# Performance work log

Hardware: AMD Instinct MI355X
Metric: run time of the kernel (lower is better)

The kernel has to match this reference:

```python
import jax, jax.numpy as jnp
import numpy as np

INPUT_DIM = 128
HIDDEN_DIM = 256
TOP_K = 512
M = 8192
N = 8192


def setup_inputs() -> dict:
    key = jax.random.key(0)
    ks = jax.random.split(key, 10)
    s_in = 1.0 / np.sqrt(INPUT_DIM)
    s_h = 1.0 / np.sqrt(HIDDEN_DIM)
    return {
        "desc0": jax.random.normal(ks[0], (1, M, INPUT_DIM), jnp.float32),
        "desc1": jax.random.normal(ks[1], (1, N, INPUT_DIM), jnp.float32),
        # mlpc0: Linear(in,h) -> ReLU -> Linear(h,h); weights stored [in,out]
        "W0a": jax.random.uniform(ks[2], (INPUT_DIM, HIDDEN_DIM), jnp.float32, -s_in, s_in),
        "b0a": jax.random.uniform(ks[3], (HIDDEN_DIM,), jnp.float32, -s_in, s_in),
        "W0b": jax.random.uniform(ks[4], (HIDDEN_DIM, HIDDEN_DIM), jnp.float32, -s_h, s_h),
        "b0b": jax.random.uniform(ks[5], (HIDDEN_DIM,), jnp.float32, -s_h, s_h),
        "W1a": jax.random.uniform(ks[6], (INPUT_DIM, HIDDEN_DIM), jnp.float32, -s_in, s_in),
        "b1a": jax.random.uniform(ks[7], (HIDDEN_DIM,), jnp.float32, -s_in, s_in),
        "W1b": jax.random.uniform(ks[8], (HIDDEN_DIM, HIDDEN_DIM), jnp.float32, -s_h, s_h),
        "b1b": jax.random.uniform(ks[9], (HIDDEN_DIM,), jnp.float32, -s_h, s_h),
    }


def _mlp(x, Wa, ba, Wb, bb):
    h = jax.nn.relu(x @ Wa + ba)
    return h @ Wb + bb


def reference(desc0, desc1, W0a, b0a, W0b, b0b, W1a, b1a, W1b, b1b):
    mdesc0 = _mlp(desc0, W0a, b0a, W0b, b0b)  # [1, M, H]
    mdesc1 = _mlp(desc1, W1a, b1a, W1b, b1b)  # [1, N, H]
    sim = jnp.einsum("bmd,bnd->bmn", mdesc0, mdesc1)  # [1, M, N]
    flat = sim[0].reshape(-1)
    _, top_idx = jax.lax.top_k(flat, TOP_K)
    n = sim.shape[2]
    rows = top_idx // n
    cols = top_idx % n
    top_k_indices_2d = jnp.stack([rows, cols], axis=1)  # [TOP_K, 2]
    return top_k_indices_2d, sim
```

## Files before the change

### kernel.cpp

```cpp
#include <hip/hip_runtime.h>
#include <stdint.h>

#define H_DIM 256
#define NCOL 8192
#define TOPK 512
#define CAND_CAP 8192

typedef unsigned short u16;
typedef __attribute__((ext_vector_type(8))) __bf16 bf16x8;
typedef __attribute__((ext_vector_type(4))) float f32x4;
typedef unsigned __attribute__((address_space(3))) lds_u32;
typedef const unsigned __attribute__((address_space(1))) glb_u32;

__device__ __forceinline__ unsigned fkey(float f) {
  unsigned u = __float_as_uint(f);
  unsigned m = (unsigned)((int)u >> 31) | 0x80000000u;
  return u ^ m;
}

__device__ __forceinline__ u16 f2bf_rne(float f) {
  unsigned u = __float_as_uint(f);
  return (u16)((u + 0x7fffu + ((u >> 16) & 1u)) >> 16);
}

__device__ __forceinline__ float bf2f(u16 h) {
  return __uint_as_float(((unsigned)h) << 16);
}

template <int K, bool RELU, bool EMIT, bool ZERO>
__global__ __launch_bounds__(256) void mlp_dual(
    const float* __restrict__ X0, const float* __restrict__ W0,
    const float* __restrict__ bias0, float* __restrict__ Y0,
    u16* __restrict__ h0, u16* __restrict__ l0,
    const float* __restrict__ X1, const float* __restrict__ W1,
    const float* __restrict__ bias1, float* __restrict__ Y1,
    u16* __restrict__ h1, u16* __restrict__ l1,
    unsigned* __restrict__ ghist, unsigned* __restrict__ counter) {
  __shared__ float Xs[16 * K];
  const int t = threadIdx.x;
  if (ZERO && blockIdx.x == 0) {
    for (int i = t; i < 4096; i += 256) ghist[i] = 0;
    if (t == 0) *counter = 0;
  }
  const int half = blockIdx.x >> 9;
  const float* X = half ? X1 : X0;
  const float* W = half ? W1 : W0;
  const float* bias = half ? bias1 : bias0;
  float* Y = half ? Y1 : Y0;
  u16* hi = half ? h1 : h0;
  u16* lo = half ? l1 : l0;
  const int row0 = (blockIdx.x & 511) * 16;

  for (int f = t; f < 4 * K; f += 256) {
    *(float4*)(Xs + f * 4) = *(const float4*)(X + (size_t)row0 * K + f * 4);
  }
  __syncthreads();
  const int cg = (t & 63) * 4;
  const int rg = (t >> 6) * 4;
  float acc[4][4];
#pragma unroll
  for (int r = 0; r < 4; r++)
#pragma unroll
    for (int c = 0; c < 4; c++) acc[r][c] = 0.f;

  for (int d = 0; d < K; d += 4) {
    float4 w0 = *(const float4*)(W + (d + 0) * H_DIM + cg);
    float4 w1 = *(const float4*)(W + (d + 1) * H_DIM + cg);
    float4 w2 = *(const float4*)(W + (d + 2) * H_DIM + cg);
    float4 w3 = *(const float4*)(W + (d + 3) * H_DIM + cg);
#pragma unroll
    for (int r = 0; r < 4; r++) {
      float4 x = *(const float4*)(Xs + (rg + r) * K + d);
#pragma unroll
      for (int c = 0; c < 4; c++) {
        float a = acc[r][c];
        a = fmaf(x.x, ((const float*)&w0)[c], a);
        a = fmaf(x.y, ((const float*)&w1)[c], a);
        a = fmaf(x.z, ((const float*)&w2)[c], a);
        a = fmaf(x.w, ((const float*)&w3)[c], a);
        acc[r][c] = a;
      }
    }
  }
  const float4 bv = *(const float4*)(bias + cg);
#pragma unroll
  for (int r = 0; r < 4; r++) {
    float4 v;
    v.x = acc[r][0] + bv.x;
    v.y = acc[r][1] + bv.y;
    v.z = acc[r][2] + bv.z;
    v.w = acc[r][3] + bv.w;
    if (RELU) {
      v.x = fmaxf(v.x, 0.f);
      v.y = fmaxf(v.y, 0.f);
      v.z = fmaxf(v.z, 0.f);
      v.w = fmaxf(v.w, 0.f);
    }
    const size_t grow = (size_t)(row0 + rg + r);
    *(float4*)(Y + grow * H_DIM + cg) = v;
    if (EMIT) {
      ushort4 hv, lv;
      hv.x = f2bf_rne(v.x); lv.x = f2bf_rne(v.x - bf2f(hv.x));
      hv.y = f2bf_rne(v.y); lv.y = f2bf_rne(v.y - bf2f(hv.y));
      hv.z = f2bf_rne(v.z); lv.z = f2bf_rne(v.z - bf2f(hv.z));
      hv.w = f2bf_rne(v.w); lv.w = f2bf_rne(v.w - bf2f(hv.w));
      *(ushort4*)(hi + grow * H_DIM + cg) = hv;
      *(ushort4*)(lo + grow * H_DIM + cg) = lv;
    }
  }
}

__global__ __launch_bounds__(512, 2) void gemm_sim_mfma(const u16* __restrict__ Ah,
                                                        const u16* __restrict__ Al,
                                                        const u16* __restrict__ Bh,
                                                        const u16* __restrict__ Bl,
                                                        float* __restrict__ C,
                                                        unsigned* __restrict__ ghist) {
  __shared__ __align__(16) char SB[131072];
  const int t = threadIdx.x;
  const int wave = t >> 6, lane = t & 63;
  const int wm = wave >> 2, wn = wave & 3;
  const int bid = blockIdx.x;
  const int swz = (bid & 7) * 128 + (bid >> 3);
  const int m0 = (swz >> 5) * 256, n0 = (swz & 31) * 256;

  f32x4 acc[8][4];
#pragma unroll
  for (int i = 0; i < 8; i++)
#pragma unroll
    for (int j = 0; j < 4; j++) acc[i][j] = (f32x4){0.f, 0.f, 0.f, 0.f};

  const int srow8 = t >> 3;
  const int sA = (t & 7) ^ (srow8 & 7);
  const u16* pAsrc = (sA < 4) ? Ah : Al;
  const u16* pBsrc = (sA < 4) ? Bh : Bl;
  const int scolE = (sA & 3) * 8;
  const int lrow = lane & 15;
  const int kq16 = (lane >> 4) << 4;
  const int asz = (lrow & 7) << 4;
  const int cH = kq16 ^ asz;
  const int cL = (64 + kq16) ^ asz;

  auto STAGE = [&](int bsel, int tt) {
    const int kofs = tt * 32;
    char* base = SB + bsel * 65536;
    const size_t ar = (size_t)(m0 + srow8) * H_DIM + kofs + scolE;
    const size_t br = (size_t)(n0 + srow8) * H_DIM + kofs + scolE;
#pragma unroll
    for (int i = 0; i < 4; i++)
      __builtin_amdgcn_global_load_lds((glb_u32*)(pAsrc + ar + (size_t)i * 64 * H_DIM),
                                       (lds_u32*)(base + i * 8192 + wave * 1024), 16, 0, 0);
#pragma unroll
    for (int i = 0; i < 4; i++)
      __builtin_amdgcn_global_load_lds((glb_u32*)(pBsrc + br + (size_t)i * 64 * H_DIM),
                                       (lds_u32*)(base + 32768 + i * 8192 + wave * 1024), 16, 0, 0);
  };

  STAGE(0, 0);
  for (int tt = 0; tt < 8; ++tt) {
    if (tt < 7) {
      STAGE((tt + 1) & 1, tt + 1);
      asm volatile("s_waitcnt vmcnt(8)" ::: "memory");
    } else {
      asm volatile("s_waitcnt vmcnt(0)" ::: "memory");
    }
    __builtin_amdgcn_s_barrier();
    asm volatile("" ::: "memory");
    const char* bb = SB + (tt & 1) * 65536;
    const char* bA = bb + (wm * 128 + lrow) * 128;
    const char* bB = bb + 32768 + (wn * 64 + lrow) * 128;
    bf16x8 aH[8], bH[4];
#pragma unroll
    for (int fm = 0; fm < 8; fm++) aH[fm] = *(const bf16x8*)(bA + fm * 2048 + cH);
#pragma unroll
    for (int fn = 0; fn < 4; fn++) bH[fn] = *(const bf16x8*)(bB + fn * 2048 + cH);
    __builtin_amdgcn_s_setprio(1);
#pragma unroll
    for (int fm = 0; fm < 8; fm++)
#pragma unroll
      for (int fn = 0; fn < 4; fn++)
        acc[fm][fn] = __builtin_amdgcn_mfma_f32_16x16x32_bf16(aH[fm], bH[fn], acc[fm][fn], 0, 0, 0);
    __builtin_amdgcn_s_setprio(0);
    {
      bf16x8 bL[4];
#pragma unroll
      for (int fn = 0; fn < 4; fn++) bL[fn] = *(const bf16x8*)(bB + fn * 2048 + cL);
      __builtin_amdgcn_s_setprio(1);
#pragma unroll
      for (int fm = 0; fm < 8; fm++)
#pragma unroll
        for (int fn = 0; fn < 4; fn++)
          acc[fm][fn] = __builtin_amdgcn_mfma_f32_16x16x32_bf16(aH[fm], bL[fn], acc[fm][fn], 0, 0, 0);
      __builtin_amdgcn_s_setprio(0);
    }
    {
      bf16x8 aL[8];
#pragma unroll
      for (int fm = 0; fm < 8; fm++) aL[fm] = *(const bf16x8*)(bA + fm * 2048 + cL);
      __builtin_amdgcn_s_setprio(1);
#pragma unroll
      for (int fm = 0; fm < 8; fm++)
#pragma unroll
        for (int fn = 0; fn < 4; fn++)
          acc[fm][fn] = __builtin_amdgcn_mfma_f32_16x16x32_bf16(aL[fm], bH[fn], acc[fm][fn], 0, 0, 0);
      __builtin_amdgcn_s_setprio(0);
    }
    __builtin_amdgcn_s_barrier();
    asm volatile("" ::: "memory");
  }

  unsigned* hist = (unsigned*)SB;
  float* Ct = (float*)(SB + 16384);
  for (int i = t; i < 4096; i += 512) hist[i] = 0;
  __syncthreads();
#pragma unroll
  for (int ch = 0; ch < 4; ++ch) {
    if (wm == (ch >> 1)) {
      const int fmb = (ch & 1) * 4;
#pragma unroll
      for (int fi = 0; fi < 4; fi++)
#pragma unroll
        for (int fn = 0; fn < 4; fn++)
#pragma unroll
          for (int q = 0; q < 4; q++)
            Ct[(fi * 16 + (lane >> 4) * 4 + q) * 260 + wn * 64 + fn * 16 + lrow] =
                acc[fmb + fi][fn][q];
    }
    __syncthreads();
#pragma unroll
    for (int u = 0; u < 8; ++u) {
      const int idx = t + u * 512;
      const int row = idx >> 6, c4 = idx & 63;
      float4 v = *(const float4*)(Ct + row * 260 + c4 * 4);
      *(float4*)(C + (size_t)(m0 + ch * 64 + row) * NCOL + n0 + c4 * 4) = v;
      atomicAdd(&hist[fkey(v.x) >> 20], 1u);
      atomicAdd(&hist[fkey(v.y) >> 20], 1u);
      atomicAdd(&hist[fkey(v.z) >> 20], 1u);
      atomicAdd(&hist[fkey(v.w) >> 20], 1u);
    }
    __syncthreads();
  }
  for (int bq = t; bq < 4096; bq += 512) {
    unsigned cc = hist[bq];
    if (cc) atomicAdd(&ghist[bq], cc);
  }
}

__global__ __launch_bounds__(256) void find_thresh(const unsigned* __restrict__ ghist,
                                                   unsigned* __restrict__ thresh) {
  __shared__ unsigned part[256];
  const int t = threadIdx.x;
  unsigned s = 0;
#pragma unroll
  for (int b = 0; b < 16; b++) s += ghist[t * 16 + b];
  part[t] = s;
  __syncthreads();
  if (t == 0) {
    unsigned cum = 0;
    int g = 255;
    for (; g > 0; g--) {
      if (cum + part[g] >= TOPK) break;
      cum += part[g];
    }
    int bsel = g * 16;
    for (int b = g * 16 + 15; b >= g * 16; b--) {
      cum += ghist[b];
      if (cum >= TOPK) { bsel = b; break; }
    }
    *thresh = (unsigned)bsel << 20;
  }
}

__device__ __forceinline__ void cand_push(unsigned kapprox, unsigned thr_m, unsigned idx,
                                          const float* __restrict__ m0f,
                                          const float* __restrict__ m1f,
                                          unsigned long long* __restrict__ cand,
                                          unsigned* __restrict__ counter) {
  if (kapprox >= thr_m) {
    const unsigned row = idx >> 13;
    const unsigned col = idx & 8191u;
    const float4* a4 = (const float4*)(m0f + (size_t)row * H_DIM);
    const float4* b4 = (const float4*)(m1f + (size_t)col * H_DIM);
    float v = 0.f;
#pragma unroll 8
    for (int k = 0; k < H_DIM / 4; k++) {
      float4 a = a4[k], b = b4[k];
      v = fmaf(a.x, b.x, v);
      v = fmaf(a.y, b.y, v);
      v = fmaf(a.z, b.z, v);
      v = fmaf(a.w, b.w, v);
    }
    unsigned p = atomicAdd(counter, 1u);
    if (p < CAND_CAP)
      cand[p] = ((unsigned long long)fkey(v) << 32) |
                (unsigned long long)(0xFFFFFFFFu - idx);
  }
}

__global__ __launch_bounds__(256) void collect(const float* __restrict__ sim,
                                               const unsigned* __restrict__ thresh,
                                               const float* __restrict__ m0f,
                                               const float* __restrict__ m1f,
                                               unsigned long long* __restrict__ cand,
                                               unsigned* __restrict__ counter) {
  const unsigned thr = *thresh;
  const unsigned thr_m = thr > 4096u ? thr - 4096u : 0u;
  const int stride = gridDim.x * blockDim.x;
  const int total4 = (NCOL * NCOL) / 4;
  const float4* s4 = (const float4*)sim;
  for (int i = blockIdx.x * blockDim.x + threadIdx.x; i < total4; i += stride) {
    float4 v = s4[i];
    unsigned base = (unsigned)i * 4u;
    cand_push(fkey(v.x), thr_m, base + 0u, m0f, m1f, cand, counter);
    cand_push(fkey(v.y), thr_m, base + 1u, m0f, m1f, cand, counter);
    cand_push(fkey(v.z), thr_m, base + 2u, m0f, m1f, cand, counter);
    cand_push(fkey(v.w), thr_m, base + 3u, m0f, m1f, cand, counter);
  }
}

__global__ __launch_bounds__(1024) void sort_topk(const unsigned long long* __restrict__ cand,
                                                  const unsigned* __restrict__ counter,
                                                  float* __restrict__ out) {
  __shared__ unsigned long long top[TOPK];
  __shared__ unsigned wred[16];
  __shared__ unsigned long long pfx_sh;
  __shared__ unsigned cnt_sh;
  const int t = threadIdx.x;
  const int n = (int)min(*counter, (unsigned)CAND_CAP);
  unsigned long long e[CAND_CAP / 1024];
#pragma unroll
  for (int u = 0; u < CAND_CAP / 1024; ++u) {
    const int i = t + u * 1024;
    e[u] = (i < n) ? cand[i] : 0ULL;
  }
  if (t == 0) cnt_sh = 0;
  __syncthreads();
  unsigned long long pfx = 0;
  for (int b = 63; b >= 0; --b) {
    const unsigned long long q = pfx | (1ULL << b);
    unsigned c = 0;
#pragma unroll
    for (int u = 0; u < CAND_CAP / 1024; ++u) c += (e[u] >= q) ? 1u : 0u;
#pragma unroll
    for (int off = 32; off; off >>= 1) c += __shfl_down(c, off, 64);
    if ((t & 63) == 0) wred[t >> 6] = c;
    __syncthreads();
    if (t == 0) {
      unsigned tot = 0;
#pragma unroll
      for (int w = 0; w < 16; ++w) tot += wred[w];
      pfx_sh = (tot >= TOPK) ? q : pfx;
    }
    __syncthreads();
    pfx = pfx_sh;
  }
#pragma unroll
  for (int u = 0; u < CAND_CAP / 1024; ++u) {
    if (e[u] >= pfx) {
      unsigned p = atomicAdd(&cnt_sh, 1u);
      if (p < TOPK) top[p] = e[u];
    }
  }
  __syncthreads();
  for (int k = 2; k <= TOPK; k <<= 1) {
    for (int j = k >> 1; j > 0; j >>= 1) {
      if (t < TOPK) {
        const int l = t ^ j;
        if (l > t) {
          const bool desc = ((t & k) == 0);
          unsigned long long a = top[t], b2 = top[l];
          if (desc ? (a < b2) : (a > b2)) { top[t] = b2; top[l] = a; }
        }
      }
      __syncthreads();
    }
  }
  if (t < TOPK) {
    const unsigned idx = 0xFFFFFFFFu - (unsigned)(top[t] & 0xFFFFFFFFull);
    out[t * 2 + 0] = (float)(idx >> 13);
    out[t * 2 + 1] = (float)(idx & 8191u);
  }
}

extern "C" void kernel_launch(void* const* d_in, const int* in_sizes, int n_in,
                              void* d_out, int out_size, void* d_ws, size_t ws_size,
                              hipStream_t stream) {
  const float* desc0 = (const float*)d_in[0];
  const float* desc1 = (const float*)d_in[1];
  const float* W0a = (const float*)d_in[2];
  const float* b0a = (const float*)d_in[3];
  const float* W0b = (const float*)d_in[4];
  const float* b0b = (const float*)d_in[5];
  const float* W1a = (const float*)d_in[6];
  const float* b1a = (const float*)d_in[7];
  const float* W1b = (const float*)d_in[8];
  const float* b1b = (const float*)d_in[9];

  char* ws = (char*)d_ws;
  unsigned* ghist = (unsigned*)ws;
  unsigned* counter = (unsigned*)(ws + 16384);
  unsigned* thresh = (unsigned*)(ws + 16388);
  unsigned long long* cand = (unsigned long long*)(ws + 16448);
  float* mdesc0f = (float*)(ws + 131072);
  float* mdesc1f = mdesc0f + 8192 * 256;
  float* hbuf0 = mdesc1f + 8192 * 256;
  float* hbuf1 = hbuf0 + 8192 * 256;
  u16* Ahh = (u16*)(hbuf1 + 8192 * 256);
  u16* All = Ahh + 8192 * 256;
  u16* Bhh = All + 8192 * 256;
  u16* Bll = Bhh + 8192 * 256;

  float* outf = (float*)d_out;
  float* sim = outf + TOPK * 2;

  mlp_dual<128, true, false, true><<<1024, 256, 0, stream>>>(
      desc0, W0a, b0a, hbuf0, nullptr, nullptr,
      desc1, W1a, b1a, hbuf1, nullptr, nullptr, ghist, counter);
  mlp_dual<256, false, true, false><<<1024, 256, 0, stream>>>(
      hbuf0, W0b, b0b, mdesc0f, Ahh, All,
      hbuf1, W1b, b1b, mdesc1f, Bhh, Bll, ghist, counter);

  gemm_sim_mfma<<<1024, 512, 0, stream>>>(Ahh, All, Bhh, Bll, sim, ghist);
  find_thresh<<<1, 256, 0, stream>>>(ghist, thresh);
  collect<<<4096, 256, 0, stream>>>(sim, thresh, mdesc0f, mdesc1f, cand, counter);
  sort_topk<<<1, 1024, 0, stream>>>(cand, counter, outf);
}
```

Before: 568.4 us.

## Fuse MLP layers, fold threshold search into collect, add GEMM barriers

The two MLP layer kernels become one kernel that keeps the hidden activations in shared memory, so the fp32 hidden buffer no longer has to be written to and read back from global memory, and one launch goes away. The single-block find_thresh kernel is removed: every collect block now recomputes the histogram threshold with a parallel suffix scan before it scans the similarity matrix. Two extra s_barrier calls are inserted between the MFMA phases of the similarity GEMM, apparently to keep waves in lockstep. In exchange, collect repeats the 4096-entry histogram read and scan in each of its 4096 blocks, and the new barriers may stall the GEMM.

```diff
diff --git a/kernel.cpp b/kernel.cpp
--- a/kernel.cpp
+++ b/kernel.cpp
@@ -27,78 +27,114 @@
   return __uint_as_float(((unsigned)h) << 16);
 }
 
-template <int K, bool RELU, bool EMIT, bool ZERO>
-__global__ __launch_bounds__(256) void mlp_dual(
-    const float* __restrict__ X0, const float* __restrict__ W0,
-    const float* __restrict__ bias0, float* __restrict__ Y0,
+__global__ __launch_bounds__(256) void mlp_fused(
+    const float* __restrict__ X0, const float* __restrict__ W0a,
+    const float* __restrict__ b0a, const float* __restrict__ W0b,
+    const float* __restrict__ b0b, float* __restrict__ Y0,
     u16* __restrict__ h0, u16* __restrict__ l0,
-    const float* __restrict__ X1, const float* __restrict__ W1,
-    const float* __restrict__ bias1, float* __restrict__ Y1,
+    const float* __restrict__ X1, const float* __restrict__ W1a,
+    const float* __restrict__ b1a, const float* __restrict__ W1b,
+    const float* __restrict__ b1b, float* __restrict__ Y1,
     u16* __restrict__ h1, u16* __restrict__ l1,
     unsigned* __restrict__ ghist, unsigned* __restrict__ counter) {
-  __shared__ float Xs[16 * K];
+  __shared__ float Xs[16 * 128];
+  __shared__ float Hs[16 * 256];
   const int t = threadIdx.x;
-  if (ZERO && blockIdx.x == 0) {
+  if (blockIdx.x == 0) {
     for (int i = t; i < 4096; i += 256) ghist[i] = 0;
     if (t == 0) *counter = 0;
   }
   const int half = blockIdx.x >> 9;
   const float* X = half ? X1 : X0;
-  const float* W = half ? W1 : W0;
-  const float* bias = half ? bias1 : bias0;
+  const float* Wa = half ? W1a : W0a;
+  const float* ba = half ? b1a : b0a;
+  const float* Wb = half ? W1b : W0b;
+  const float* bb_ = half ? b1b : b0b;
   float* Y = half ? Y1 : Y0;
   u16* hi = half ? h1 : h0;
   u16* lo = half ? l1 : l0;
   const int row0 = (blockIdx.x & 511) * 16;
 
-  for (int f = t; f < 4 * K; f += 256) {
-    *(float4*)(Xs + f * 4) = *(const float4*)(X + (size_t)row0 * K + f * 4);
+  for (int f = t; f < 512; f += 256) {
+    *(float4*)(Xs + f * 4) = *(const float4*)(X + (size_t)row0 * 128 + f * 4);
   }
   __syncthreads();
   const int cg = (t & 63) * 4;
   const int rg = (t >> 6) * 4;
-  float acc[4][4];
-#pragma unroll
-  for (int r = 0; r < 4; r++)
-#pragma unroll
-    for (int c = 0; c < 4; c++) acc[r][c] = 0.f;
-
-  for (int d = 0; d < K; d += 4) {
-    float4 w0 = *(const float4*)(W + (d + 0) * H_DIM + cg);
-    float4 w1 = *(const float4*)(W + (d + 1) * H_DIM + cg);
-    float4 w2 = *(const float4*)(W + (d + 2) * H_DIM + cg);
-    float4 w3 = *(const float4*)(W + (d + 3) * H_DIM + cg);
+
+  {
+    float acc[4][4];
+#pragma unroll
+    for (int r = 0; r < 4; r++)
+#pragma unroll
+      for (int c = 0; c < 4; c++) acc[r][c] = 0.f;
+    for (int d = 0; d < 128; d += 4) {
+      float4 w0 = *(const float4*)(Wa + (d + 0) * H_DIM + cg);
+      float4 w1 = *(const float4*)(Wa + (d + 1) * H_DIM + cg);
+      float4 w2 = *(const float4*)(Wa + (d + 2) * H_DIM + cg);
+      float4 w3 = *(const float4*)(Wa + (d + 3) * H_DIM + cg);
+#pragma unroll
+      for (int r = 0; r < 4; r++) {
+        float4 x = *(const float4*)(Xs + (rg + r) * 128 + d);
+#pragma unroll
+        for (int c = 0; c < 4; c++) {
+          float a = acc[r][c];
+          a = fmaf(x.x, ((const float*)&w0)[c], a);
+          a = fmaf(x.y, ((const float*)&w1)[c], a);
+          a = fmaf(x.z, ((const float*)&w2)[c], a);
+          a = fmaf(x.w, ((const float*)&w3)[c], a);
+          acc[r][c] = a;
+        }
+      }
+    }
+    const float4 bv = *(const float4*)(ba + cg);
 #pragma unroll
     for (int r = 0; r < 4; r++) {
-      float4 x = *(const float4*)(Xs + (rg + r) * K + d);
-#pragma unroll
-      for (int c = 0; c < 4; c++) {
-        float a = acc[r][c];
-        a = fmaf(x.x, ((const float*)&w0)[c], a);
-        a = fmaf(x.y, ((const float*)&w1)[c], a);
-        a = fmaf(x.z, ((const float*)&w2)[c], a);
-        a = fmaf(x.w, ((const float*)&w3)[c], a);
-        acc[r][c] = a;
+      float4 v;
+      v.x = fmaxf(acc[r][0] + bv.x, 0.f);
+      v.y = fmaxf(acc[r][1] + bv.y, 0.f);
+      v.z = fmaxf(acc[r][2] + bv.z, 0.f);
+      v.w = fmaxf(acc[r][3] + bv.w, 0.f);
+      *(float4*)(Hs + (rg + r) * 256 + cg) = v;
+    }
+  }
+  __syncthreads();
+
+  {
+    float acc[4][4];
+#pragma unroll
+    for (int r = 0; r < 4; r++)
+#pragma unroll
+      for (int c = 0; c < 4; c++) acc[r][c] = 0.f;
+    for (int d = 0; d < 256; d += 4) {
+      float4 w0 = *(const float4*)(Wb + (d + 0) * H_DIM + cg);
+      float4 w1 = *(const float4*)(Wb + (d + 1) * H_DIM + cg);
+      float4 w2 = *(const float4*)(Wb + (d + 2) * H_DIM + cg);
+      float4 w3 = *(const float4*)(Wb + (d + 3) * H_DIM + cg);
+#pragma unroll
+      for (int r = 0; r < 4; r++) {
+        float4 x = *(const float4*)(Hs + (rg + r) * 256 + d);
+#pragma unroll
+        for (int c = 0; c < 4; c++) {
+          float a = acc[r][c];
+          a = fmaf(x.x, ((const float*)&w0)[c], a);
+          a = fmaf(x.y, ((const float*)&w1)[c], a);
+          a = fmaf(x.z, ((const float*)&w2)[c], a);
+          a = fmaf(x.w, ((const float*)&w3)[c], a);
+          acc[r][c] = a;
+        }
       }
     }
-  }
-  const float4 bv = *(const float4*)(bias + cg);
-#pragma unroll
-  for (int r = 0; r < 4; r++) {
-    float4 v;
-    v.x = acc[r][0] + bv.x;
-    v.y = acc[r][1] + bv.y;
-    v.z = acc[r][2] + bv.z;
-    v.w = acc[r][3] + bv.w;
-    if (RELU) {
-      v.x = fmaxf(v.x, 0.f);
-      v.y = fmaxf(v.y, 0.f);
-      v.z = fmaxf(v.z, 0.f);
-      v.w = fmaxf(v.w, 0.f);
-    }
-    const size_t grow = (size_t)(row0 + rg + r);
-    *(float4*)(Y + grow * H_DIM + cg) = v;
-    if (EMIT) {
+    const float4 bv = *(const float4*)(bb_ + cg);
+#pragma unroll
+    for (int r = 0; r < 4; r++) {
+      float4 v;
+      v.x = acc[r][0] + bv.x;
+      v.y = acc[r][1] + bv.y;
+      v.z = acc[r][2] + bv.z;
+      v.w = acc[r][3] + bv.w;
+      const size_t grow = (size_t)(row0 + rg + r);
+      *(float4*)(Y + grow * H_DIM + cg) = v;
       ushort4 hv, lv;
       hv.x = f2bf_rne(v.x); lv.x = f2bf_rne(v.x - bf2f(hv.x));
       hv.y = f2bf_rne(v.y); lv.y = f2bf_rne(v.y - bf2f(hv.y));
@@ -169,6 +205,7 @@
     const char* bb = SB + (tt & 1) * 65536;
     const char* bA = bb + (wm * 128 + lrow) * 128;
     const char* bB = bb + 32768 + (wn * 64 + lrow) * 128;
+
     bf16x8 aH[8], bH[4];
 #pragma unroll
     for (int fm = 0; fm < 8; fm++) aH[fm] = *(const bf16x8*)(bA + fm * 2048 + cH);
@@ -181,6 +218,8 @@
       for (int fn = 0; fn < 4; fn++)
         acc[fm][fn] = __builtin_amdgcn_mfma_f32_16x16x32_bf16(aH[fm], bH[fn], acc[fm][fn], 0, 0, 0);
     __builtin_amdgcn_s_setprio(0);
+    __builtin_amdgcn_s_barrier();
+
     {
       bf16x8 bL[4];
 #pragma unroll
@@ -193,6 +232,8 @@
           acc[fm][fn] = __builtin_amdgcn_mfma_f32_16x16x32_bf16(aH[fm], bL[fn], acc[fm][fn], 0, 0, 0);
       __builtin_amdgcn_s_setprio(0);
     }
+    __builtin_amdgcn_s_barrier();
+
     {
       bf16x8 aL[8];
 #pragma unroll
@@ -243,31 +284,6 @@
   for (int bq = t; bq < 4096; bq += 512) {
     unsigned cc = hist[bq];
     if (cc) atomicAdd(&ghist[bq], cc);
-  }
-}
-
-__global__ __launch_bounds__(256) void find_thresh(const unsigned* __restrict__ ghist,
-                                                   unsigned* __restrict__ thresh) {
-  __shared__ unsigned part[256];
-  const int t = threadIdx.x;
-  unsigned s = 0;
-#pragma unroll
-  for (int b = 0; b < 16; b++) s += ghist[t * 16 + b];
-  part[t] = s;
-  __syncthreads();
-  if (t == 0) {
-    unsigned cum = 0;
-    int g = 255;
-    for (; g > 0; g--) {
-      if (cum + part[g] >= TOPK) break;
-      cum += part[g];
-    }
-    int bsel = g * 16;
-    for (int b = g * 16 + 15; b >= g * 16; b--) {
-      cum += ghist[b];
-      if (cum >= TOPK) { bsel = b; break; }
-    }
-    *thresh = (unsigned)bsel << 20;
   }
 }
 
@@ -298,12 +314,38 @@
 }
 
 __global__ __launch_bounds__(256) void collect(const float* __restrict__ sim,
-                                               const unsigned* __restrict__ thresh,
+                                               const unsigned* __restrict__ ghist,
                                                const float* __restrict__ m0f,
                                                const float* __restrict__ m1f,
                                                unsigned long long* __restrict__ cand,
                                                unsigned* __restrict__ counter) {
-  const unsigned thr = *thresh;
+  __shared__ unsigned part[256];
+  __shared__ unsigned thr_sh;
+  const int t = threadIdx.x;
+  {
+    unsigned s = 0;
+#pragma unroll
+    for (int b = 0; b < 16; b++) s += ghist[t * 16 + b];
+    part[t] = s;
+    __syncthreads();
+    for (int off = 1; off < 256; off <<= 1) {
+      unsigned v = part[t] + ((t + off < 256) ? part[t + off] : 0u);
+      __syncthreads();
+      part[t] = v;
+      __syncthreads();
+    }
+    if (part[t] >= TOPK && (t == 255 || part[t + 1] < TOPK)) {
+      unsigned cum = (t == 255) ? 0u : part[t + 1];
+      int bsel = t * 16;
+      for (int b = t * 16 + 15; b >= t * 16; --b) {
+        cum += ghist[b];
+        if (cum >= TOPK) { bsel = b; break; }
+      }
+      thr_sh = (unsigned)bsel << 20;
+    }
+    __syncthreads();
+  }
+  const unsigned thr = thr_sh;
   const unsigned thr_m = thr > 4096u ? thr - 4096u : 0u;
   const int stride = gridDim.x * blockDim.x;
   const int total4 = (NCOL * NCOL) / 4;
@@ -399,13 +441,10 @@
   char* ws = (char*)d_ws;
   unsigned* ghist = (unsigned*)ws;
   unsigned* counter = (unsigned*)(ws + 16384);
-  unsigned* thresh = (unsigned*)(ws + 16388);
   unsigned long long* cand = (unsigned long long*)(ws + 16448);
   float* mdesc0f = (float*)(ws + 131072);
   float* mdesc1f = mdesc0f + 8192 * 256;
-  float* hbuf0 = mdesc1f + 8192 * 256;
-  float* hbuf1 = hbuf0 + 8192 * 256;
-  u16* Ahh = (u16*)(hbuf1 + 8192 * 256);
+  u16* Ahh = (u16*)(mdesc1f + 8192 * 256);
   u16* All = Ahh + 8192 * 256;
   u16* Bhh = All + 8192 * 256;
   u16* Bll = Bhh + 8192 * 256;
@@ -413,15 +452,11 @@
   float* outf = (float*)d_out;
   float* sim = outf + TOPK * 2;
 
-  mlp_dual<128, true, false, true><<<1024, 256, 0, stream>>>(
-      desc0, W0a, b0a, hbuf0, nullptr, nullptr,
-      desc1, W1a, b1a, hbuf1, nullptr, nullptr, ghist, counter);
-  mlp_dual<256, false, true, false><<<1024, 256, 0, stream>>>(
-      hbuf0, W0b, b0b, mdesc0f, Ahh, All,
-      hbuf1, W1b, b1b, mdesc1f, Bhh, Bll, ghist, counter);
+  mlp_fused<<<1024, 256, 0, stream>>>(
+      desc0, W0a, b0a, W0b, b0b, mdesc0f, Ahh, All,
+      desc1, W1a, b1a, W1b, b1b, mdesc1f, Bhh, Bll, ghist, counter);
 
   gemm_sim_mfma<<<1024, 512, 0, stream>>>(Ahh, All, Bhh, Bll, sim, ghist);
-  find_thresh<<<1, 256, 0, stream>>>(ghist, thresh);
-  collect<<<4096, 256, 0, stream>>>(sim, thresh, mdesc0f, mdesc1f, cand, counter);
+  collect<<<4096, 256, 0, stream>>>(sim, ghist, mdesc0f, mdesc1f, cand, counter);
   sort_topk<<<1, 1024, 0, stream>>>(cand, counter, outf);
 }
```

Measured after the change: 544.9 us. 1.04x faster.
